# Optimization experiments

Hardware: AMD Instinct MI355X
Metric: run time of the kernel (lower is better)

## Reference

```python
import jax, jax.numpy as jnp
import numpy as np
from jax import lax

BN_EPS = 1e-3


def fps(xyz, npoint):
    """Farthest point sampling. xyz: (B,N,3) -> idx: (B, npoint) int32.
    Deterministic start at index 0 (torch version uses randint)."""
    B, N, _ = xyz.shape
    batch = jnp.arange(B)

    def step(carry, _):
        dist, farthest = carry                      # (B,N), (B,)
        centroid = xyz[batch, farthest]             # (B,3)
        d = jnp.sum((xyz - centroid[:, None, :]) ** 2, axis=-1)  # (B,N)
        dist = jnp.minimum(dist, d)
        nxt = jnp.argmax(dist, axis=-1)
        return (dist, nxt), farthest

    init = (jnp.full((B, N), 1e10, dtype=xyz.dtype), jnp.zeros((B,), dtype=jnp.int32))
    _, idx = lax.scan(step, init, None, length=npoint)  # (npoint, B)
    return idx.T                                        # (B, npoint)


def _bn(y, g, b, m, v):
    # eval-mode BatchNorm1d over channel axis (last)
    return (y - m) * (g * lax.rsqrt(v + BN_EPS)) + b


def setup_inputs() -> dict:
    key = jax.random.key(0)
    ks = jax.random.split(key, 16)
    B, N, C, S = 32, 8192, 64, 512
    cin, cout, hid = 3 + C, 2 * C, 8  # hidden = max(8, 128//16)
    xyz = jax.random.normal(ks[0], (B, N, 3), jnp.float32)
    feat = jax.random.normal(ks[1], (B, N, C), jnp.float32)
    sc = lambda fan: 1.0 / np.sqrt(fan)
    return {
        "xyz": xyz,
        "feat": feat,
        "W1": jax.random.normal(ks[2], (cout, cin), jnp.float32) * sc(cin),
        "g1": jnp.ones((cout,), jnp.float32),
        "b1": jnp.zeros((cout,), jnp.float32),
        "m1": jax.random.normal(ks[3], (cout,), jnp.float32) * 0.1,
        "v1": jax.random.uniform(ks[4], (cout,), jnp.float32) + 0.5,
        "W2": jax.random.normal(ks[5], (cout, cout), jnp.float32) * sc(cout),
        "g2": jnp.ones((cout,), jnp.float32),
        "b2": jnp.zeros((cout,), jnp.float32),
        "m2": jax.random.normal(ks[6], (cout,), jnp.float32) * 0.1,
        "v2": jax.random.uniform(ks[7], (cout,), jnp.float32) + 0.5,
        "Wproj": jax.random.normal(ks[8], (cout, cin), jnp.float32) * sc(cin),
        "Wse1": jax.random.normal(ks[9], (hid, cout), jnp.float32) * sc(cout),
        "bse1": jnp.zeros((hid,), jnp.float32),
        "Wse2": jax.random.normal(ks[10], (cout, hid), jnp.float32) * sc(hid),
        "bse2": jnp.zeros((cout,), jnp.float32),
        "npoint": S,
    }


def reference(xyz, feat, W1, g1, b1, m1, v1, W2, g2, b2, m2, v2,
              Wproj, Wse1, bse1, Wse2, bse2, npoint):
    # FPS + gather (the irregular-access part)
    idx = fps(xyz, npoint)                                     # (B,S)
    xyz_s = jnp.take_along_axis(xyz, idx[..., None], axis=1)   # (B,S,3)
    feat_s = jnp.take_along_axis(feat, idx[..., None], axis=1) # (B,S,C)
    x = jnp.concatenate([xyz_s, feat_s], axis=-1)              # (B,S,cin)

    # ResMLP1D: conv1x1 -> BN -> ReLU -> conv1x1 -> BN, then SE, residual, ReLU
    h = jax.nn.relu(_bn(jnp.einsum('bsc,oc->bso', x, W1), g1, b1, m1, v1))
    h = _bn(jnp.einsum('bsc,oc->bso', h, W2), g2, b2, m2, v2)  # (B,S,cout)

    # SE1D: global average pool over points, 2-layer bottleneck, sigmoid gate
    s = h.mean(axis=1)                                         # (B,cout)
    s = jax.nn.relu(s @ Wse1.T + bse1)
    s = jax.nn.sigmoid(s @ Wse2.T + bse2)
    h = h * s[:, None, :]

    out = jax.nn.relu(h + jnp.einsum('bsc,oc->bso', x, Wproj))
    return out
```

## Files before the change

### kernel.cpp

```cpp
#include <hip/hip_runtime.h>
#include <math.h>

#define B_ 32
#define N_ 8192
#define C_ 64
#define S_ 512
#define CIN 67
#define COUT 128

template <int CTRL>
__device__ __forceinline__ unsigned dppmov(unsigned v) {
  return (unsigned)__builtin_amdgcn_update_dpp(0, (int)v, CTRL, 0xF, 0xF, true);
}
template <int CTRL>
__device__ __forceinline__ float dppmaxf(float v) {
  return fmaxf(v, __uint_as_float(dppmov<CTRL>(__float_as_uint(v))));
}

__global__ __launch_bounds__(256)
void fps_kernel(const float* __restrict__ xyz, int* __restrict__ idx_out) {
  __shared__ float lx[N_], ly[N_], lz[N_];
  __shared__ unsigned long long slotbuf[2][4];
  __shared__ int idxl[S_];
  const int b = blockIdx.x;
  const int t = threadIdx.x;
  const float* base = xyz + (size_t)b * N_ * 3;
  #pragma unroll
  for (int k = 0; k < 24; ++k) {
    int j = k * 256 + t;
    float4 v = ((const float4*)base)[j];
    int f = j * 4;
    float vals[4] = {v.x, v.y, v.z, v.w};
    #pragma unroll
    for (int e = 0; e < 4; ++e) {
      int ff = f + e;
      int p = ff / 3;
      int c = ff - p * 3;
      if (c == 0) lx[p] = vals[e];
      else if (c == 1) ly[p] = vals[e];
      else lz[p] = vals[e];
    }
  }
  __syncthreads();
  const int p0 = t * 32;
  float px[32], py[32], pz[32], dist[32];
  #pragma unroll
  for (int j = 0; j < 32; ++j) {
    px[j] = lx[p0 + j];
    py[j] = ly[p0 + j];
    pz[j] = lz[p0 + j];
    dist[j] = 1e10f;
  }
  #pragma unroll
  for (int j = 0; j < 32; ++j)
    asm volatile("" : "+v"(px[j]), "+v"(py[j]), "+v"(pz[j]));

  int bidx = 0;
  float cx = lx[0], cy = ly[0], cz = lz[0];
  const int w = t >> 6;
  const int lane = t & 63;

  for (int s = 0; s < S_; ++s) {
    const int par = s & 1;
    if (t == 0) idxl[s] = bidx;
    float gv[4];
    int gi[4];
    #pragma unroll
    for (int g = 0; g < 4; ++g) {
      gv[g] = -1.0f;
      gi[g] = 0;
      #pragma unroll
      for (int u = 0; u < 8; ++u) {
        const int j = g * 8 + u;
        float dx = __fsub_rn(px[j], cx);
        float dy = __fsub_rn(py[j], cy);
        float dz = __fsub_rn(pz[j], cz);
        float d = __fadd_rn(__fadd_rn(__fmul_rn(dx, dx), __fmul_rn(dy, dy)),
                            __fmul_rn(dz, dz));
        d = fminf(dist[j], d);
        dist[j] = d;
        if (d > gv[g]) { gv[g] = d; gi[g] = j; }
      }
    }
    float bestv = gv[0];
    int bj = gi[0];
    #pragma unroll
    for (int g = 1; g < 4; ++g)
      if (gv[g] > bestv) { bestv = gv[g]; bj = gi[g]; }
    float m = bestv;
    m = dppmaxf<0x111>(m);
    m = dppmaxf<0x112>(m);
    m = dppmaxf<0x114>(m);
    m = dppmaxf<0x118>(m);
    m = dppmaxf<0x142>(m);
    m = dppmaxf<0x143>(m);
    const float M = __uint_as_float(
        (unsigned)__builtin_amdgcn_readlane((int)__float_as_uint(m), 63));
    const unsigned long long ball = __ballot(bestv == M);
    const int l0 = __ffsll(ball) - 1;
    const int bj0 = __builtin_amdgcn_readlane(bj, l0);
    const int widx = ((w << 6) | l0) * 32 + bj0;
    if (lane == 63)
      slotbuf[par][w] =
          ((unsigned long long)__float_as_uint(M) << 32) | (unsigned)(8191 - widx);
    __syncthreads();
    unsigned long long best = slotbuf[par][0];
    #pragma unroll
    for (int w2 = 1; w2 < 4; ++w2) {
      unsigned long long k2 = slotbuf[par][w2];
      if (k2 > best) best = k2;
    }
    bidx = 8191 - (int)(unsigned)(best & 0xFFFFFFFFull);
    cx = lx[bidx]; cy = ly[bidx]; cz = lz[bidx];
  }
  for (int i = t; i < S_; i += 256) idx_out[b * S_ + i] = idxl[i];
}

__global__ __launch_bounds__(256) void mlp_kernel(
    const float* __restrict__ xyz, const float* __restrict__ feat,
    const float* __restrict__ W1, const float* __restrict__ g1,
    const float* __restrict__ b1, const float* __restrict__ m1,
    const float* __restrict__ v1, const float* __restrict__ W2,
    const float* __restrict__ g2, const float* __restrict__ b2,
    const float* __restrict__ m2, const float* __restrict__ v2,
    const float* __restrict__ Wproj, const int* __restrict__ idx,
    float* __restrict__ h2buf, float* __restrict__ partials,
    float* __restrict__ projbuf) {
  __shared__ float xs[CIN][64];
  __shared__ float hs[COUT][64];
  __shared__ float wlds[COUT][COUT];
  __shared__ float psums[8][COUT];
  const int blk = blockIdx.x;
  const int b = blk >> 3, tile = blk & 7;
  const int t = threadIdx.x;

  {
    const int p = t >> 2, q = t & 3;
    const int pid = idx[b * S_ + tile * 64 + p];
    const float* frow = feat + ((size_t)(b * N_ + pid)) * C_ + q * 16;
    #pragma unroll
    for (int i = 0; i < 4; ++i) {
      float4 v = ((const float4*)frow)[i];
      xs[3 + q * 16 + i * 4 + 0][p] = v.x;
      xs[3 + q * 16 + i * 4 + 1][p] = v.y;
      xs[3 + q * 16 + i * 4 + 2][p] = v.z;
      xs[3 + q * 16 + i * 4 + 3][p] = v.w;
    }
    if (q == 0) {
      const float* xr = xyz + ((size_t)(b * N_ + pid)) * 3;
      xs[0][p] = xr[0]; xs[1][p] = xr[1]; xs[2][p] = xr[2];
    }
  }
  for (int f = t; f < COUT * CIN; f += 256) {
    int o = f / CIN, k = f - o * CIN;
    wlds[k][o] = W1[f];
  }
  __syncthreads();

  const int py = t >> 5, ox = t & 31;
  const int py8 = py * 8, ox4 = ox * 4;
  float acc[8][4];

  #pragma unroll
  for (int i = 0; i < 8; ++i)
    #pragma unroll
    for (int j = 0; j < 4; ++j) acc[i][j] = 0.0f;
  for (int k = 0; k < CIN; ++k) {
    float4 xa = *(const float4*)&xs[k][py8];
    float4 xb = *(const float4*)&xs[k][py8 + 4];
    float4 wv = *(const float4*)&wlds[k][ox4];
    float xv[8] = {xa.x, xa.y, xa.z, xa.w, xb.x, xb.y, xb.z, xb.w};
    float wr[4] = {wv.x, wv.y, wv.z, wv.w};
    #pragma unroll
    for (int i = 0; i < 8; ++i)
      #pragma unroll
      for (int j = 0; j < 4; ++j) acc[i][j] = fmaf(xv[i], wr[j], acc[i][j]);
  }
  #pragma unroll
  for (int j = 0; j < 4; ++j) {
    const int o = ox4 + j;
    const float sc = g1[o] * (1.0f / sqrtf(v1[o] + 1e-3f));
    const float sh = b1[o] - m1[o] * sc;
    #pragma unroll
    for (int i = 0; i < 8; ++i)
      hs[o][py8 + i] = fmaxf(fmaf(acc[i][j], sc, sh), 0.0f);
  }
  __syncthreads();
  for (int f = t; f < COUT * COUT; f += 256) {
    int o = f >> 7, k = f & 127;
    wlds[k][o] = W2[f];
  }
  __syncthreads();

  #pragma unroll
  for (int i = 0; i < 8; ++i)
    #pragma unroll
    for (int j = 0; j < 4; ++j) acc[i][j] = 0.0f;
  for (int k = 0; k < COUT; ++k) {
    float4 xa = *(const float4*)&hs[k][py8];
    float4 xb = *(const float4*)&hs[k][py8 + 4];
    float4 wv = *(const float4*)&wlds[k][ox4];
    float xv[8] = {xa.x, xa.y, xa.z, xa.w, xb.x, xb.y, xb.z, xb.w};
    float wr[4] = {wv.x, wv.y, wv.z, wv.w};
    #pragma unroll
    for (int i = 0; i < 8; ++i)
      #pragma unroll
      for (int j = 0; j < 4; ++j) acc[i][j] = fmaf(xv[i], wr[j], acc[i][j]);
  }
  {
    float sc[4], sh[4], sume[4];
    #pragma unroll
    for (int j = 0; j < 4; ++j) {
      const int o = ox4 + j;
      sc[j] = g2[o] * (1.0f / sqrtf(v2[o] + 1e-3f));
      sh[j] = b2[o] - m2[o] * sc[j];
      sume[j] = 0.0f;
    }
    const int basept = b * S_ + tile * 64 + py8;
    #pragma unroll
    for (int i = 0; i < 8; ++i) {
      float4 hv;
      hv.x = fmaf(acc[i][0], sc[0], sh[0]);
      hv.y = fmaf(acc[i][1], sc[1], sh[1]);
      hv.z = fmaf(acc[i][2], sc[2], sh[2]);
      hv.w = fmaf(acc[i][3], sc[3], sh[3]);
      sume[0] += hv.x; sume[1] += hv.y; sume[2] += hv.z; sume[3] += hv.w;
      *(float4*)&h2buf[((size_t)(basept + i)) * COUT + ox4] = hv;
    }
    *(float4*)&psums[py][ox4] = make_float4(sume[0], sume[1], sume[2], sume[3]);
  }
  __syncthreads();
  if (t < COUT) {
    float sacc = 0.0f;
    #pragma unroll
    for (int r = 0; r < 8; ++r) sacc += psums[r][t];
    partials[(b * 8 + tile) * COUT + t] = sacc;
  }
  for (int f = t; f < COUT * CIN; f += 256) {
    int o = f / CIN, k = f - o * CIN;
    wlds[k][o] = Wproj[f];
  }
  __syncthreads();

  #pragma unroll
  for (int i = 0; i < 8; ++i)
    #pragma unroll
    for (int j = 0; j < 4; ++j) acc[i][j] = 0.0f;
  for (int k = 0; k < CIN; ++k) {
    float4 xa = *(const float4*)&xs[k][py8];
    float4 xb = *(const float4*)&xs[k][py8 + 4];
    float4 wv = *(const float4*)&wlds[k][ox4];
    float xv[8] = {xa.x, xa.y, xa.z, xa.w, xb.x, xb.y, xb.z, xb.w};
    float wr[4] = {wv.x, wv.y, wv.z, wv.w};
    #pragma unroll
    for (int i = 0; i < 8; ++i)
      #pragma unroll
      for (int j = 0; j < 4; ++j) acc[i][j] = fmaf(xv[i], wr[j], acc[i][j]);
  }
  {
    const int basept = b * S_ + tile * 64 + py8;
    #pragma unroll
    for (int i = 0; i < 8; ++i) {
      float4 pv = make_float4(acc[i][0], acc[i][1], acc[i][2], acc[i][3]);
      *(float4*)&projbuf[((size_t)(basept + i)) * COUT + ox4] = pv;
    }
  }
}

__global__ __launch_bounds__(128) void se_kernel(
    const float* __restrict__ partials, const float* __restrict__ Wse1,
    const float* __restrict__ bse1, const float* __restrict__ Wse2,
    const float* __restrict__ bse2, float* __restrict__ sgate) {
  __shared__ float mv[COUT];
  __shared__ float rv[8];
  const int b = blockIdx.x;
  const int t = threadIdx.x;
  float s = 0.0f;
  #pragma unroll
  for (int r = 0; r < 8; ++r) s += partials[(b * 8 + r) * COUT + t];
  mv[t] = s * (1.0f / (float)S_);
  __syncthreads();
  if (t < 8) {
    float a = bse1[t];
    for (int o = 0; o < COUT; ++o) a = fmaf(mv[o], Wse1[t * COUT + o], a);
    rv[t] = fmaxf(a, 0.0f);
  }
  __syncthreads();
  float a = bse2[t];
  #pragma unroll
  for (int h = 0; h < 8; ++h) a = fmaf(rv[h], Wse2[t * 8 + h], a);
  sgate[b * COUT + t] = 1.0f / (1.0f + expf(-a));
}

__global__ __launch_bounds__(256) void finish_kernel(
    const float* __restrict__ h2buf, const float* __restrict__ sgate,
    float* __restrict__ out) {
  const int i = blockIdx.x * 256 + threadIdx.x;
  const int total = B_ * S_ * COUT / 4;
  if (i >= total) return;
  const int fo = i & 31;
  const int row = i >> 5;
  const int b = row >> 9;
  float4 h = ((const float4*)h2buf)[i];
  float4 g = ((const float4*)sgate)[b * 32 + fo];
  float4 p = ((float4*)out)[i];
  float4 r;
  r.x = fmaxf(fmaf(h.x, g.x, p.x), 0.0f);
  r.y = fmaxf(fmaf(h.y, g.y, p.y), 0.0f);
  r.z = fmaxf(fmaf(h.z, g.z, p.z), 0.0f);
  r.w = fmaxf(fmaf(h.w, g.w, p.w), 0.0f);
  ((float4*)out)[i] = r;
}

extern "C" void kernel_launch(void* const* d_in, const int* in_sizes, int n_in,
                              void* d_out, int out_size, void* d_ws, size_t ws_size,
                              hipStream_t stream) {
  const float* xyz   = (const float*)d_in[0];
  const float* feat  = (const float*)d_in[1];
  const float* W1    = (const float*)d_in[2];
  const float* g1    = (const float*)d_in[3];
  const float* b1    = (const float*)d_in[4];
  const float* m1    = (const float*)d_in[5];
  const float* v1    = (const float*)d_in[6];
  const float* W2    = (const float*)d_in[7];
  const float* g2    = (const float*)d_in[8];
  const float* b2    = (const float*)d_in[9];
  const float* m2    = (const float*)d_in[10];
  const float* v2    = (const float*)d_in[11];
  const float* Wproj = (const float*)d_in[12];
  const float* Wse1  = (const float*)d_in[13];
  const float* bse1  = (const float*)d_in[14];
  const float* Wse2  = (const float*)d_in[15];
  const float* bse2  = (const float*)d_in[16];
  float* out = (float*)d_out;

  char* ws = (char*)d_ws;
  int*   idx      = (int*)ws;
  float* h2buf    = (float*)(ws + (64 << 10));
  float* partials = (float*)(ws + (64 << 10) + B_ * S_ * COUT * 4);
  float* sgate    = (float*)(ws + (64 << 10) + B_ * S_ * COUT * 4 +
                             B_ * 8 * COUT * 4);

  fps_kernel<<<B_, 256, 0, stream>>>(xyz, idx);
  mlp_kernel<<<B_ * 8, 256, 0, stream>>>(xyz, feat, W1, g1, b1, m1, v1,
                                         W2, g2, b2, m2, v2, Wproj, idx,
                                         h2buf, partials, out);
  se_kernel<<<B_, 128, 0, stream>>>(partials, Wse1, bse1, Wse2, bse2, sgate);
  finish_kernel<<<(B_ * S_ * COUT / 4 + 255) / 256, 256, 0, stream>>>(h2buf, sgate, out);
}
```

Baseline: 525.1 us.

## Double FPS block to 512 threads and simplify cross-wave argmax reduction

The FPS kernel now runs 512 threads per batch (8 waves), each thread owning 16 points instead of 32. This halves the serial per-thread distance work in each of the 512 sequential iterations. The packed 64-bit slot reduction is replaced by separate max and index arrays read as vectors, with first-index tie breaking. In exchange there are more waves to synchronise at each barrier, and the asm register pinning is removed.

```diff
diff --git a/kernel.cpp b/kernel.cpp
--- a/kernel.cpp
+++ b/kernel.cpp
@@ -17,17 +17,18 @@
   return fmaxf(v, __uint_as_float(dppmov<CTRL>(__float_as_uint(v))));
 }
 
-__global__ __launch_bounds__(256)
+__global__ __launch_bounds__(512)
 void fps_kernel(const float* __restrict__ xyz, int* __restrict__ idx_out) {
   __shared__ float lx[N_], ly[N_], lz[N_];
-  __shared__ unsigned long long slotbuf[2][4];
+  __shared__ __align__(16) float sM[2][8];
+  __shared__ __align__(16) int sI[2][8];
   __shared__ int idxl[S_];
   const int b = blockIdx.x;
   const int t = threadIdx.x;
   const float* base = xyz + (size_t)b * N_ * 3;
   #pragma unroll
-  for (int k = 0; k < 24; ++k) {
-    int j = k * 256 + t;
+  for (int k = 0; k < 12; ++k) {
+    int j = k * 512 + t;
     float4 v = ((const float4*)base)[j];
     int f = j * 4;
     float vals[4] = {v.x, v.y, v.z, v.w};
@@ -42,19 +43,15 @@
     }
   }
   __syncthreads();
-  const int p0 = t * 32;
-  float px[32], py[32], pz[32], dist[32];
-  #pragma unroll
-  for (int j = 0; j < 32; ++j) {
+  const int p0 = t * 16;
+  float px[16], py[16], pz[16], dist[16];
+  #pragma unroll
+  for (int j = 0; j < 16; ++j) {
     px[j] = lx[p0 + j];
     py[j] = ly[p0 + j];
     pz[j] = lz[p0 + j];
     dist[j] = 1e10f;
   }
-  #pragma unroll
-  for (int j = 0; j < 32; ++j)
-    asm volatile("" : "+v"(px[j]), "+v"(py[j]), "+v"(pz[j]));
-
   int bidx = 0;
   float cx = lx[0], cy = ly[0], cz = lz[0];
   const int w = t >> 6;
@@ -63,10 +60,10 @@
   for (int s = 0; s < S_; ++s) {
     const int par = s & 1;
     if (t == 0) idxl[s] = bidx;
-    float gv[4];
-    int gi[4];
-    #pragma unroll
-    for (int g = 0; g < 4; ++g) {
+    float gv[2];
+    int gi[2];
+    #pragma unroll
+    for (int g = 0; g < 2; ++g) {
       gv[g] = -1.0f;
       gi[g] = 0;
       #pragma unroll
@@ -84,9 +81,7 @@
     }
     float bestv = gv[0];
     int bj = gi[0];
-    #pragma unroll
-    for (int g = 1; g < 4; ++g)
-      if (gv[g] > bestv) { bestv = gv[g]; bj = gi[g]; }
+    if (gv[1] > bestv) { bestv = gv[1]; bj = gi[1]; }
     float m = bestv;
     m = dppmaxf<0x111>(m);
     m = dppmaxf<0x112>(m);
@@ -99,21 +94,27 @@
     const unsigned long long ball = __ballot(bestv == M);
     const int l0 = __ffsll(ball) - 1;
     const int bj0 = __builtin_amdgcn_readlane(bj, l0);
-    const int widx = ((w << 6) | l0) * 32 + bj0;
-    if (lane == 63)
-      slotbuf[par][w] =
-          ((unsigned long long)__float_as_uint(M) << 32) | (unsigned)(8191 - widx);
+    const int widx = ((w << 6) | l0) * 16 + bj0;
+    if (lane == 0) { sM[par][w] = M; sI[par][w] = widx; }
     __syncthreads();
-    unsigned long long best = slotbuf[par][0];
-    #pragma unroll
-    for (int w2 = 1; w2 < 4; ++w2) {
-      unsigned long long k2 = slotbuf[par][w2];
-      if (k2 > best) best = k2;
-    }
-    bidx = 8191 - (int)(unsigned)(best & 0xFFFFFFFFull);
+    const float4 ma = *(const float4*)&sM[par][0];
+    const float4 mb = *(const float4*)&sM[par][4];
+    const int4 ia = *(const int4*)&sI[par][0];
+    const int4 ib = *(const int4*)&sI[par][4];
+    const float mm = fmaxf(fmaxf(fmaxf(ma.x, ma.y), fmaxf(ma.z, ma.w)),
+                           fmaxf(fmaxf(mb.x, mb.y), fmaxf(mb.z, mb.w)));
+    int nb = ib.w;
+    nb = (mb.z == mm) ? ib.z : nb;
+    nb = (mb.y == mm) ? ib.y : nb;
+    nb = (mb.x == mm) ? ib.x : nb;
+    nb = (ma.w == mm) ? ia.w : nb;
+    nb = (ma.z == mm) ? ia.z : nb;
+    nb = (ma.y == mm) ? ia.y : nb;
+    nb = (ma.x == mm) ? ia.x : nb;
+    bidx = nb;
     cx = lx[bidx]; cy = ly[bidx]; cz = lz[bidx];
   }
-  for (int i = t; i < S_; i += 256) idx_out[b * S_ + i] = idxl[i];
+  if (t < S_) idx_out[b * S_ + t] = idxl[t];
 }
 
 __global__ __launch_bounds__(256) void mlp_kernel(
@@ -341,7 +342,7 @@
   float* sgate    = (float*)(ws + (64 << 10) + B_ * S_ * COUT * 4 +
                              B_ * 8 * COUT * 4);
 
-  fps_kernel<<<B_, 256, 0, stream>>>(xyz, idx);
+  fps_kernel<<<B_, 512, 0, stream>>>(xyz, idx);
   mlp_kernel<<<B_ * 8, 256, 0, stream>>>(xyz, feat, W1, g1, b1, m1, v1,
                                          W2, g2, b2, m2, v2, Wproj, idx,
                                          h2buf, partials, out);
```

New measurement: 532.4 us. Within noise of the previous version (+1.4%).

## Split FPS per batch across four cooperating blocks with global-memory spin sync

Applied to the files above, without the earlier changes.

Each batch's farthest point sampling now runs on four workgroups instead of one. Each workgroup owns a quarter of the points, with 8 points per thread instead of 32. Every iteration, each wave publishes a key packing the step number, the max distance and the index to a global slot array, then spins until all 16 slots show the current step. This cuts per-step arithmetic and raises device occupancy from 32 blocks, at the cost of a global-memory round trip per step. It relies on all 128 blocks being co-resident to avoid deadlock, and it adds a memset launch.

```diff
diff --git a/kernel.cpp b/kernel.cpp
--- a/kernel.cpp
+++ b/kernel.cpp
@@ -7,6 +7,8 @@
 #define S_ 512
 #define CIN 67
 #define COUT 128
+#define MEMB 4
+#define PTS 8
 
 template <int CTRL>
 __device__ __forceinline__ unsigned dppmov(unsigned v) {
@@ -18,11 +20,13 @@
 }
 
 __global__ __launch_bounds__(256)
-void fps_kernel(const float* __restrict__ xyz, int* __restrict__ idx_out) {
+void fps_kernel(const float* __restrict__ xyz, int* __restrict__ idx_out,
+                unsigned long long* __restrict__ gslots) {
   __shared__ float lx[N_], ly[N_], lz[N_];
-  __shared__ unsigned long long slotbuf[2][4];
   __shared__ int idxl[S_];
-  const int b = blockIdx.x;
+  const int blk = blockIdx.x;
+  const int b = blk & 31;
+  const int m = blk >> 5;
   const int t = threadIdx.x;
   const float* base = xyz + (size_t)b * N_ * 3;
   #pragma unroll
@@ -42,36 +46,34 @@
     }
   }
   __syncthreads();
-  const int p0 = t * 32;
-  float px[32], py[32], pz[32], dist[32];
-  #pragma unroll
-  for (int j = 0; j < 32; ++j) {
+  const int p0 = m * (N_ / MEMB) + t * PTS;
+  float px[PTS], py[PTS], pz[PTS], dist[PTS];
+  #pragma unroll
+  for (int j = 0; j < PTS; ++j) {
     px[j] = lx[p0 + j];
     py[j] = ly[p0 + j];
     pz[j] = lz[p0 + j];
     dist[j] = 1e10f;
   }
-  #pragma unroll
-  for (int j = 0; j < 32; ++j)
-    asm volatile("" : "+v"(px[j]), "+v"(py[j]), "+v"(pz[j]));
-
+  unsigned long long* slots = gslots + b * (2 * 4 * MEMB);
+  const int w = t >> 6;
+  const int lane = t & 63;
+  const int myslot = (m << 2) | w;
   int bidx = 0;
   float cx = lx[0], cy = ly[0], cz = lz[0];
-  const int w = t >> 6;
-  const int lane = t & 63;
 
   for (int s = 0; s < S_; ++s) {
     const int par = s & 1;
-    if (t == 0) idxl[s] = bidx;
-    float gv[4];
-    int gi[4];
-    #pragma unroll
-    for (int g = 0; g < 4; ++g) {
+    if (m == 0 && t == 0) idxl[s] = bidx;
+    float gv[2];
+    int gi[2];
+    #pragma unroll
+    for (int g = 0; g < 2; ++g) {
       gv[g] = -1.0f;
       gi[g] = 0;
       #pragma unroll
-      for (int u = 0; u < 8; ++u) {
-        const int j = g * 8 + u;
+      for (int u = 0; u < 4; ++u) {
+        const int j = g * 4 + u;
         float dx = __fsub_rn(px[j], cx);
         float dy = __fsub_rn(py[j], cy);
         float dz = __fsub_rn(pz[j], cz);
@@ -84,36 +86,51 @@
     }
     float bestv = gv[0];
     int bj = gi[0];
-    #pragma unroll
-    for (int g = 1; g < 4; ++g)
-      if (gv[g] > bestv) { bestv = gv[g]; bj = gi[g]; }
-    float m = bestv;
-    m = dppmaxf<0x111>(m);
-    m = dppmaxf<0x112>(m);
-    m = dppmaxf<0x114>(m);
-    m = dppmaxf<0x118>(m);
-    m = dppmaxf<0x142>(m);
-    m = dppmaxf<0x143>(m);
+    if (gv[1] > bestv) { bestv = gv[1]; bj = gi[1]; }
+    float mx = bestv;
+    mx = dppmaxf<0x111>(mx);
+    mx = dppmaxf<0x112>(mx);
+    mx = dppmaxf<0x114>(mx);
+    mx = dppmaxf<0x118>(mx);
+    mx = dppmaxf<0x142>(mx);
+    mx = dppmaxf<0x143>(mx);
     const float M = __uint_as_float(
-        (unsigned)__builtin_amdgcn_readlane((int)__float_as_uint(m), 63));
+        (unsigned)__builtin_amdgcn_readlane((int)__float_as_uint(mx), 63));
     const unsigned long long ball = __ballot(bestv == M);
     const int l0 = __ffsll(ball) - 1;
     const int bj0 = __builtin_amdgcn_readlane(bj, l0);
-    const int widx = ((w << 6) | l0) * 32 + bj0;
-    if (lane == 63)
-      slotbuf[par][w] =
-          ((unsigned long long)__float_as_uint(M) << 32) | (unsigned)(8191 - widx);
+    const int widx = m * (N_ / MEMB) + ((w << 6) | l0) * PTS + bj0;
+    const float Mc = M < 0.0f ? 0.0f : M;
+    const unsigned long long key =
+        ((unsigned long long)(s + 1) << 46) |
+        ((unsigned long long)__float_as_uint(Mc) << 14) |
+        (unsigned long long)(16383 - widx);
+    if (lane == 0)
+      __hip_atomic_store(&slots[par * 16 + myslot], key, __ATOMIC_RELAXED,
+                         __HIP_MEMORY_SCOPE_AGENT);
+    const unsigned long long want = (unsigned long long)(s + 1) << 46;
+    unsigned long long kk[16];
+    unsigned long long mis;
+    do {
+      mis = 0;
+      #pragma unroll
+      for (int q = 0; q < 16; ++q) {
+        kk[q] = __hip_atomic_load(&slots[par * 16 + q], __ATOMIC_RELAXED,
+                                  __HIP_MEMORY_SCOPE_AGENT);
+        mis |= (kk[q] ^ want) >> 46;
+      }
+    } while (mis != 0);
+    unsigned long long best = kk[0];
+    #pragma unroll
+    for (int q = 1; q < 16; ++q)
+      if (kk[q] > best) best = kk[q];
+    bidx = 16383 - (int)(unsigned)(best & 0x3FFFull);
+    cx = lx[bidx]; cy = ly[bidx]; cz = lz[bidx];
+  }
+  if (m == 0) {
     __syncthreads();
-    unsigned long long best = slotbuf[par][0];
-    #pragma unroll
-    for (int w2 = 1; w2 < 4; ++w2) {
-      unsigned long long k2 = slotbuf[par][w2];
-      if (k2 > best) best = k2;
-    }
-    bidx = 8191 - (int)(unsigned)(best & 0xFFFFFFFFull);
-    cx = lx[bidx]; cy = ly[bidx]; cz = lz[bidx];
-  }
-  for (int i = t; i < S_; i += 256) idx_out[b * S_ + i] = idxl[i];
+    for (int i = t; i < S_; i += 256) idx_out[b * S_ + i] = idxl[i];
+  }
 }
 
 __global__ __launch_bounds__(256) void mlp_kernel(
@@ -337,11 +354,13 @@
   char* ws = (char*)d_ws;
   int*   idx      = (int*)ws;
   float* h2buf    = (float*)(ws + (64 << 10));
-  float* partials = (float*)(ws + (64 << 10) + B_ * S_ * COUT * 4);
-  float* sgate    = (float*)(ws + (64 << 10) + B_ * S_ * COUT * 4 +
-                             B_ * 8 * COUT * 4);
-
-  fps_kernel<<<B_, 256, 0, stream>>>(xyz, idx);
+  float* partials = (float*)(ws + 8454144);
+  float* sgate    = (float*)(ws + 8585216);
+  unsigned long long* gslots = (unsigned long long*)(ws + 8601600);
+
+  hipMemsetAsync(gslots, 0, B_ * 2 * 4 * MEMB * sizeof(unsigned long long),
+                 stream);
+  fps_kernel<<<B_ * MEMB, 256, 0, stream>>>(xyz, idx, gslots);
   mlp_kernel<<<B_ * 8, 256, 0, stream>>>(xyz, feat, W1, g1, b1, m1, v1,
                                          W2, g2, b2, m2, v2, Wproj, idx,
                                          h2buf, partials, out);
```

Result: slower. 1.276 ms (+143.1%).
